# Optimization experiments

Hardware: AMD Instinct MI355X
Metric: run time of the kernel (lower is better)

The kernel has to match this reference:

```python
import jax, jax.numpy as jnp
import numpy as np

KC = 32      # cluster_num
KS = 3       # kernel_size
AREA = KS * KS
ITERS = 10   # KMeans Lloyd iterations (fixed, deterministic init)


def _unfold3(x):
    # torch nn.Unfold(kernel_size=3, padding=1): feature dim ordered cin-major, area-minor
    b, c, h, w = x.shape
    xp = jnp.pad(x, ((0, 0), (0, 0), (1, 1), (1, 1)))
    cols = jnp.stack([xp[:, :, i:i + h, j:j + w] for i in range(KS) for j in range(KS)], axis=2)  # [b,c,area,h,w]
    return cols.reshape(b, c * AREA, h * w).transpose(0, 2, 1)  # [b, hw, c*area]


def _kmeans_assign(feat):
    # Lloyd's KMeans on [s, d] features; deterministic strided init; returns [s] int assignments
    s, d = feat.shape
    c0 = feat[jnp.arange(KC) * (s // KC)]
    f2 = (feat * feat).sum(-1, keepdims=True)
    def dists(c):
        return f2 - 2.0 * feat @ c.T + (c * c).sum(-1)[None, :]
    def step(c, _):
        idx = jnp.argmin(dists(c), axis=1)
        cnt = jax.ops.segment_sum(jnp.ones((s,), feat.dtype), idx, KC)
        sm = jax.ops.segment_sum(feat, idx, KC)
        c_new = jnp.where(cnt[:, None] > 0, sm / jnp.maximum(cnt, 1.0)[:, None], c)
        return c_new, None
    c, _ = jax.lax.scan(step, c0, None, length=ITERS)
    return jnp.argmin(dists(c), axis=1)


def _seg_mean(p, idx):
    # per-cluster mean of patches -> patch-space centroids [K, f]
    s = p.shape[0]
    cnt = jax.ops.segment_sum(jnp.ones((s,), p.dtype), idx, KC)
    return jax.ops.segment_sum(p, idx, KC) / jnp.maximum(cnt, 1.0)[:, None]


def _mlp2(x, W1, b1, W2, b2):
    return jax.nn.relu(jax.nn.relu(x @ W1 + b1) @ W2 + b2)


def setup_inputs():
    key = jax.random.key(0)
    ks = jax.random.split(key, 16)
    cin, cout, m = 32, 32, 16
    f = cin * AREA
    g = lambda k, shp, sc: jax.random.normal(k, shp, dtype=jnp.float32) * sc
    return {
        "x": g(ks[0], (4, cin, 64, 64), 1.0),
        "Wh1": g(ks[1], (f, m), (2.0 / f) ** 0.5), "bh1": jnp.zeros((m,), jnp.float32),
        "Wh2": g(ks[2], (m, m), (2.0 / m) ** 0.5), "bh2": jnp.zeros((m,), jnp.float32),
        "Wa": g(ks[3], (m, AREA), (2.0 / m) ** 0.5), "ba": jnp.zeros((AREA,), jnp.float32),
        "Wc": g(ks[4], (m, cin), (2.0 / m) ** 0.5), "bc": jnp.zeros((cin,), jnp.float32),
        "Wo": g(ks[5], (m, cout), (2.0 / m) ** 0.5), "bo": jnp.zeros((cout,), jnp.float32),
        "kernels": g(ks[6], (cin, AREA, cout), (2.0 / (cin * AREA)) ** 0.5),
        "Wb1": g(ks[7], (f, m), (2.0 / f) ** 0.5), "bb1": jnp.zeros((m,), jnp.float32),
        "Wb2": g(ks[8], (m, m), (2.0 / m) ** 0.5), "bb2": jnp.zeros((m,), jnp.float32),
        "Wb3": g(ks[9], (m, cout), (2.0 / m) ** 0.5), "bb3": jnp.zeros((cout,), jnp.float32),
    }


def reference(x, Wh1, bh1, Wh2, bh2, Wa, ba, Wc, bc, Wo, bo, kernels, Wb1, bb1, Wb2, bb2, Wb3, bb3):
    b, cin, h, w = x.shape
    s = h * w
    cout = kernels.shape[-1]
    patches = _unfold3(x)                                        # [b, s, cin*area]
    feat = patches.reshape(b, s, cin, AREA).mean(-1)             # cluster_source='channel'
    idx = jax.vmap(_kmeans_assign)(jax.lax.stop_gradient(feat))  # [b, s] cluster assignments
    centroids = jax.vmap(_seg_mean)(patches, idx)                # [b, K, cin*area]
    # low_rank kernel generator: rank-1 modulation along cin/area/cout of shared base kernel
    kf = _mlp2(centroids, Wh1, bh1, Wh2, bh2)                    # [b, K, m]
    w_cin = jax.nn.sigmoid(kf @ Wc + bc)                         # [b, K, cin]
    w_area = jax.nn.sigmoid(kf @ Wa + ba)                        # [b, K, area]
    w_cout = jax.nn.sigmoid(kf @ Wo + bo)                        # [b, K, cout]
    kern = (w_cin[:, :, :, None, None] * w_area[:, :, None, :, None]
            * w_cout[:, :, None, None, :] * kernels[None, None])  # [b, K, cin, area, cout]
    kern = kern.reshape(b, KC, cin * AREA, cout)
    bias = _mlp2(centroids, Wb1, bb1, Wb2, bb2) @ Wb3 + bb3      # [b, K, cout] (bias='cluster')
    # gather per-pixel kernel/bias by cluster id, grouped matmul, scatter back (dense-gather form)
    bi = jnp.arange(b)[:, None]
    Wpix = kern[bi, idx]                                         # [b, s, f, cout]
    out = jnp.einsum('bsf,bsfo->bso', patches, Wpix) + bias[bi, idx]
    return out.reshape(b, h, w, cout).transpose(0, 3, 1, 2), idx
```

## Files before the change

kernel.cpp:

```cpp
#include <hip/hip_runtime.h>
#include <stdint.h>

typedef unsigned long long u64;

#define Bn 4
#define CINn 32
#define Hn 64
#define Wn 64
#define Sn 4096
#define KCn 32
#define Mn 16
#define COUTn 32
#define AREAn 9
#define Fn 288
#define NITER 10
#define FXSCALE 4294967296.0
#define SPLITn 4

static __device__ __forceinline__ float relu_(float v){ return v > 0.f ? v : 0.f; }
static __device__ __forceinline__ float sigm_(float v){ return 1.f / (1.f + __expf(-v) * 0.f + expf(-v) * 1.f); }
static __device__ __forceinline__ float sigmoid_(float v){ return 1.f / (1.f + expf(-v)); }

__global__ __launch_bounds__(256) void k_feat(const float* __restrict__ x,
                                              float* __restrict__ feat,
                                              u64* __restrict__ gsum,
                                              unsigned* __restrict__ gcnt){
    int g = blockIdx.x * 256 + threadIdx.x;
    if (g < 3 * Bn * KCn * CINn) gsum[g] = 0ull;
    if (g < 3 * Bn * KCn)        gcnt[g] = 0u;
    int p = g & (Sn - 1);
    int c = (g >> 12) & (CINn - 1);
    int b = g >> 17;
    int y = p >> 6, xx = p & 63;
    const float* xc = x + ((size_t)(b * CINn + c) << 12);
    float s = 0.f;
    #pragma unroll
    for (int i = 0; i < 3; ++i){
        int yy = y + i - 1;
        if (yy < 0 || yy >= Hn) continue;
        #pragma unroll
        for (int j = 0; j < 3; ++j){
            int xj = xx + j - 1;
            if (xj < 0 || xj >= Wn) continue;
            s += xc[(yy << 6) + xj];
        }
    }
    feat[g] = s * (1.f / 9.f);
}

__global__ __launch_bounds__(256) void k_assign(const float* __restrict__ feat,
                                                float* __restrict__ gcent,
                                                u64* __restrict__ gsum,
                                                unsigned* __restrict__ gcnt,
                                                int* __restrict__ idx,
                                                float* __restrict__ idxf,
                                                int iter){
    __shared__ float cent[KCn][CINn];
    __shared__ float c2[KCn];
    __shared__ u64   lsum[KCn][CINn];
    __shared__ unsigned lcnt[KCn];

    int tid  = threadIdx.x;
    int b    = blockIdx.x >> 4;
    int tile = blockIdx.x & 15;
    int prev = (iter + 2) % 3;
    int cur  = iter % 3;
    int nxt  = (iter + 1) % 3;

    for (int e = tid; e < KCn * CINn; e += 256){
        int k = e >> 5, c = e & 31;
        float v;
        if (iter == 0){
            v = feat[(b * CINn + c) * Sn + k * (Sn / KCn)];
        } else {
            u64 svu     = gsum[((prev * Bn + b) * KCn + k) * CINn + c];
            unsigned cn = gcnt[(prev * Bn + b) * KCn + k];
            if (cn > 0) v = (float)((double)(long long)svu / ((double)cn * FXSCALE));
            else        v = gcent[(b * KCn + k) * CINn + c];
        }
        cent[k][c] = v;
        lsum[k][c] = 0ull;
        if (tile == 0){
            gcent[(b * KCn + k) * CINn + c] = v;
            gsum[((nxt * Bn + b) * KCn + k) * CINn + c] = 0ull;
        }
    }
    for (int e = tid; e < KCn; e += 256){
        lcnt[e] = 0u;
        if (tile == 0) gcnt[(nxt * Bn + b) * KCn + e] = 0u;
    }
    __syncthreads();
    if (tid < KCn){
        float s = 0.f;
        #pragma unroll
        for (int c = 0; c < CINn; ++c) s += cent[tid][c] * cent[tid][c];
        c2[tid] = s;
    }
    __syncthreads();

    int p = (tile << 8) | tid;
    float fv[CINn];
    #pragma unroll
    for (int c = 0; c < CINn; ++c) fv[c] = feat[(b * CINn + c) * Sn + p];
    float f2 = 0.f;
    #pragma unroll
    for (int c = 0; c < CINn; ++c) f2 = fmaf(fv[c], fv[c], f2);

    float best = 3.402823466e38f; int bi = 0;
    #pragma unroll 4
    for (int k = 0; k < KCn; ++k){
        float dot = 0.f;
        #pragma unroll
        for (int c = 0; c < CINn; ++c) dot = fmaf(fv[c], cent[k][c], dot);
        float d = f2 - 2.f * dot + c2[k];
        if (d < best){ best = d; bi = k; }
    }

    if (iter == NITER){
        idx[b * Sn + p]  = bi;
        idxf[b * Sn + p] = (float)bi;
        return;
    }

    atomicAdd(&lcnt[bi], 1u);
    #pragma unroll
    for (int c = 0; c < CINn; ++c){
        long long q = llrint((double)fv[c] * FXSCALE);
        atomicAdd(&lsum[bi][c], (u64)q);
    }
    __syncthreads();
    for (int e = tid; e < KCn * CINn; e += 256){
        int k = e >> 5, c = e & 31;
        u64 v = lsum[k][c];
        if (v) atomicAdd(&gsum[((cur * Bn + b) * KCn + k) * CINn + c], v);
    }
    if (tid < KCn){
        unsigned v = lcnt[tid];
        if (v) atomicAdd(&gcnt[(cur * Bn + b) * KCn + tid], v);
    }
}

__global__ __launch_bounds__(256) void k_sort(const int* __restrict__ idx,
                                              int* __restrict__ sorted,
                                              int* __restrict__ offs){
    int b = blockIdx.x, tid = threadIdx.x;
    __shared__ unsigned hist[256][KCn];
    __shared__ unsigned cnts[KCn];
    __shared__ unsigned baseK[KCn + 1];
    #pragma unroll
    for (int k = 0; k < KCn; ++k) hist[tid][k] = 0u;
    int p0 = tid * 16;
    int myk[16];
    #pragma unroll
    for (int i = 0; i < 16; ++i){
        int k = idx[b * Sn + p0 + i];
        myk[i] = k;
        hist[tid][k]++;
    }
    __syncthreads();
    if (tid < KCn){
        unsigned run = 0;
        for (int t = 0; t < 256; ++t){ unsigned v = hist[t][tid]; hist[t][tid] = run; run += v; }
        cnts[tid] = run;
    }
    __syncthreads();
    if (tid == 0){
        unsigned acc = 0;
        for (int k = 0; k < KCn; ++k){ baseK[k] = acc; acc += cnts[k]; }
        baseK[KCn] = acc;
    }
    __syncthreads();
    if (tid <= KCn) offs[b * (KCn + 1) + tid] = (int)baseK[tid];
    #pragma unroll
    for (int i = 0; i < 16; ++i){
        int k = myk[i];
        unsigned pos = baseK[k] + hist[tid][k];
        hist[tid][k]++;
        sorted[b * Sn + pos] = p0 + i;
    }
}

__global__ __launch_bounds__(320) void k_segsum(const float* __restrict__ x,
                                                const int* __restrict__ sorted,
                                                const int* __restrict__ offs,
                                                float* __restrict__ centp){
    int bk = blockIdx.x; int b = bk >> 5; int k = bk & 31;
    int tid = threadIdx.x;
    int f = tid < Fn ? tid : (Fn - 1);
    int off0 = offs[b * (KCn + 1) + k];
    int n    = offs[b * (KCn + 1) + k + 1] - off0;
    int c = f / 9, a = f - c * 9;
    int di = a / 3 - 1, dj = a % 3 - 1;
    const float* xc = x + ((size_t)(b * CINn + c) << 12);
    const int* plist = sorted + b * Sn + off0;
    __shared__ int pl[320];
    float sum = 0.f;
    for (int base = 0; base < n; base += 320){
        int m = min(320, n - base);
        __syncthreads();
        if (tid < m) pl[tid] = plist[base + tid];
        __syncthreads();
        #pragma unroll 4
        for (int i = 0; i < m; ++i){
            int p = pl[i];
            int y = (p >> 6) + di, xx = (p & 63) + dj;
            float v = (y >= 0 && y < Hn && xx >= 0 && xx < Wn) ? xc[(y << 6) + xx] : 0.f;
            sum += v;
        }
    }
    if (tid < Fn) centp[(b * KCn + k) * Fn + f] = sum / (float)max(n, 1);
}

__global__ __launch_bounds__(512) void k_mlp(const float* __restrict__ centp,
        const float* __restrict__ Wh1, const float* __restrict__ bh1,
        const float* __restrict__ Wh2, const float* __restrict__ bh2,
        const float* __restrict__ Wa,  const float* __restrict__ ba,
        const float* __restrict__ Wc,  const float* __restrict__ bc,
        const float* __restrict__ Wo,  const float* __restrict__ bo,
        const float* __restrict__ Wb1, const float* __restrict__ bb1,
        const float* __restrict__ Wb2, const float* __restrict__ bb2,
        const float* __restrict__ Wb3, const float* __restrict__ bb3,
        float* __restrict__ wcin, float* __restrict__ warea,
        float* __restrict__ wcout, float* __restrict__ biasb){
    int b = blockIdx.x, tid = threadIdx.x;
    int k = tid >> 4, j = tid & 15;
    __shared__ float centL[KCn * Fn];
    __shared__ float h1[KCn][Mn], hb1s[KCn][Mn];
    __shared__ float kf[KCn][Mn], hb2[KCn][Mn];
    for (int e = tid; e < KCn * Fn; e += 512) centL[e] = centp[b * KCn * Fn + e];
    __syncthreads();
    {
        float a1 = bh1[j], a2 = bb1[j];
        const float* cr = centL + k * Fn;
        for (int f = 0; f < Fn; ++f){
            float cv = cr[f];
            a1 = fmaf(cv, Wh1[f * Mn + j], a1);
            a2 = fmaf(cv, Wb1[f * Mn + j], a2);
        }
        h1[k][j]   = relu_(a1);
        hb1s[k][j] = relu_(a2);
    }
    __syncthreads();
    {
        float a1 = bh2[j], a2 = bb2[j];
        #pragma unroll
        for (int i = 0; i < Mn; ++i){
            a1 = fmaf(h1[k][i],   Wh2[i * Mn + j], a1);
            a2 = fmaf(hb1s[k][i], Wb2[i * Mn + j], a2);
        }
        kf[k][j]  = relu_(a1);
        hb2[k][j] = relu_(a2);
    }
    __syncthreads();
    for (int e = tid; e < KCn * COUTn; e += 512){
        int kk = e >> 5, o = e & 31;
        float s1 = bc[o], s2 = bo[o], s3 = bb3[o];
        #pragma unroll
        for (int i = 0; i < Mn; ++i){
            float kv = kf[kk][i];
            s1 = fmaf(kv, Wc[i * COUTn + o], s1);
            s2 = fmaf(kv, Wo[i * COUTn + o], s2);
            s3 = fmaf(hb2[kk][i], Wb3[i * COUTn + o], s3);
        }
        wcin [(b * KCn + kk) * CINn  + o] = sigmoid_(s1);
        wcout[(b * KCn + kk) * COUTn + o] = sigmoid_(s2);
        biasb[(b * KCn + kk) * COUTn + o] = s3;
    }
    if (tid < KCn * AREAn){
        int kk = tid / 9, a = tid - kk * 9;
        float s = ba[a];
        #pragma unroll
        for (int i = 0; i < Mn; ++i) s = fmaf(kf[kk][i], Wa[i * AREAn + a], s);
        warea[(b * KCn + kk) * AREAn + a] = sigmoid_(s);
    }
}

__global__ __launch_bounds__(256) void k_out(const float* __restrict__ x,
                                             const int* __restrict__ sorted,
                                             const int* __restrict__ offs,
                                             const float* __restrict__ wcin,
                                             const float* __restrict__ warea,
                                             const float* __restrict__ wcout,
                                             const float* __restrict__ biasb,
                                             const float* __restrict__ kern0,
                                             float* __restrict__ out){
    int g  = blockIdx.x;
    int sp = g & (SPLITn - 1);
    int k  = (g >> 2) & 31;
    int b  = g >> 7;
    int tid = threadIdx.x;

    __shared__ float kernT[COUTn][292];
    __shared__ float biasL[COUTn];
    __shared__ float wcl[CINn], wal[16], wol[COUTn];
    __shared__ float patchL[8 * Fn];
    __shared__ int   pix[8];

    if (tid < 32)                 wcl[tid]       = wcin [(b * KCn + k) * CINn  + tid];
    else if (tid < 64)            wol[tid - 32]  = wcout[(b * KCn + k) * COUTn + tid - 32];
    else if (tid < 64 + AREAn)    wal[tid - 64]  = warea[(b * KCn + k) * AREAn + tid - 64];
    else if (tid >= 96 && tid < 128) biasL[tid - 96] = biasb[(b * KCn + k) * COUTn + tid - 96];
    __syncthreads();

    for (int e = tid; e < Fn * COUTn; e += 256){
        int f = e >> 5, o = e & 31;
        int c = f / 9, a = f - c * 9;
        kernT[o][f] = wcl[c] * wal[a] * wol[o] * kern0[e];
    }

    int off0 = offs[b * (KCn + 1) + k];
    int n    = offs[b * (KCn + 1) + k + 1] - off0;
    int per  = (n + SPLITn - 1) >> 2;
    int i0 = sp * per, i1 = min(n, i0 + per);
    __syncthreads();

    for (int base = i0; base < i1; base += 8){
        int m = min(8, i1 - base);
        if (tid < 8) pix[tid] = (tid < m) ? sorted[b * Sn + off0 + base + tid] : -1;
        __syncthreads();
        for (int v = tid; v < 8 * Fn; v += 256){
            int pl = v / Fn, f = v - pl * Fn;
            int p = pix[pl];
            float val = 0.f;
            if (p >= 0){
                int c = f / 9, a = f - c * 9;
                int y = (p >> 6) + a / 3 - 1, xx = (p & 63) + (a % 3) - 1;
                if (y >= 0 && y < Hn && xx >= 0 && xx < Wn)
                    val = x[((size_t)(b * CINn + c) << 12) + (y << 6) + xx];
            }
            patchL[v] = val;
        }
        __syncthreads();
        int pl = tid >> 5, o = tid & 31;
        if (pl < m){
            const float* pr = patchL + pl * Fn;
            const float* kr = &kernT[o][0];
            float a0 = 0.f, a1 = 0.f, a2 = 0.f, a3 = 0.f;
            #pragma unroll
            for (int f = 0; f < Fn; f += 4){
                float4 pv = *reinterpret_cast<const float4*>(pr + f);
                float4 kv = *reinterpret_cast<const float4*>(kr + f);
                a0 = fmaf(pv.x, kv.x, a0);
                a1 = fmaf(pv.y, kv.y, a1);
                a2 = fmaf(pv.z, kv.z, a2);
                a3 = fmaf(pv.w, kv.w, a3);
            }
            float acc = biasL[o] + ((a0 + a1) + (a2 + a3));
            out[((size_t)(b * COUTn + o) << 12) + pix[pl]] = acc;
        }
        __syncthreads();
    }
}

extern "C" void kernel_launch(void* const* d_in, const int* in_sizes, int n_in,
                              void* d_out, int out_size, void* d_ws, size_t ws_size,
                              hipStream_t stream){
    const float* x    = (const float*)d_in[0];
    const float* Wh1  = (const float*)d_in[1];
    const float* bh1  = (const float*)d_in[2];
    const float* Wh2  = (const float*)d_in[3];
    const float* bh2  = (const float*)d_in[4];
    const float* Wa   = (const float*)d_in[5];
    const float* ba   = (const float*)d_in[6];
    const float* Wc   = (const float*)d_in[7];
    const float* bc   = (const float*)d_in[8];
    const float* Wo   = (const float*)d_in[9];
    const float* bo   = (const float*)d_in[10];
    const float* kern0= (const float*)d_in[11];
    const float* Wb1  = (const float*)d_in[12];
    const float* bb1  = (const float*)d_in[13];
    const float* Wb2  = (const float*)d_in[14];
    const float* bb2  = (const float*)d_in[15];
    const float* Wb3  = (const float*)d_in[16];
    const float* bb3  = (const float*)d_in[17];

    char* ws = (char*)d_ws;
    float*    feat   = (float*)(ws + 0);
    float*    gcent  = (float*)(ws + 2097152);
    u64*      gsum   = (u64*)  (ws + 2113536);
    unsigned* gcnt   = (unsigned*)(ws + 2211840);
    int*      idx    = (int*)  (ws + 2213376);
    int*      sorted = (int*)  (ws + 2278912);
    int*      offs   = (int*)  (ws + 2344448);
    float*    centp  = (float*)(ws + 2345216);
    float*    wcin   = (float*)(ws + 2492672);
    float*    warea  = (float*)(ws + 2509056);
    float*    wcout  = (float*)(ws + 2513664);
    float*    biasb  = (float*)(ws + 2530048);

    float* outp = (float*)d_out;
    float* idxf = outp + (size_t)Bn * COUTn * Sn;

    k_feat<<<(Bn * CINn * Sn) / 256, 256, 0, stream>>>(x, feat, gsum, gcnt);
    for (int it = 0; it <= NITER; ++it)
        k_assign<<<Bn * 16, 256, 0, stream>>>(feat, gcent, gsum, gcnt, idx, idxf, it);
    k_sort<<<Bn, 256, 0, stream>>>(idx, sorted, offs);
    k_segsum<<<Bn * KCn, 320, 0, stream>>>(x, sorted, offs, centp);
    k_mlp<<<Bn, 512, 0, stream>>>(centp, Wh1, bh1, Wh2, bh2, Wa, ba, Wc, bc, Wo, bo,
                                  Wb1, bb1, Wb2, bb2, Wb3, bb3,
                                  wcin, warea, wcout, biasb);
    k_out<<<Bn * KCn * SPLITn, 256, 0, stream>>>(x, sorted, offs, wcin, warea, wcout,
                                                 biasb, kern0, outp);
}
```

Baseline: 248.2 us.

## Fuse KMeans iterations, sort, segsum and MLP into one persistent kernel with grid barriers

The separate per-iteration assign launches, the sort, the segment-sum and the MLP kernels are merged into one persistent kernel with 32 blocks per batch. The blocks synchronise through a software atomic barrier, which removes about 14 kernel launches and their serialization gaps. The per-cluster sums are now built in shared memory by bucketing pixels into lists rather than doing 64-bit shared atomics per channel, and each block splits the 32 centroid distance checks across two half-blocks. The output kernel is retiled to fixed 32-pixel tiles with 2x2 register blocking and rebuilds the kernel for each cluster run, which risks redundant kernel builds and depends on all blocks being co-resident for the spin barrier.

```diff
diff --git a/kernel.cpp b/kernel.cpp
--- a/kernel.cpp
+++ b/kernel.cpp
@@ -15,19 +15,39 @@
 #define Fn 288
 #define NITER 10
 #define FXSCALE 4294967296.0
-#define SPLITn 4
+#define NBLK_B 32
+#define LDK 292
 
 static __device__ __forceinline__ float relu_(float v){ return v > 0.f ? v : 0.f; }
-static __device__ __forceinline__ float sigm_(float v){ return 1.f / (1.f + __expf(-v) * 0.f + expf(-v) * 1.f); }
 static __device__ __forceinline__ float sigmoid_(float v){ return 1.f / (1.f + expf(-v)); }
 
-__global__ __launch_bounds__(256) void k_feat(const float* __restrict__ x,
+static __device__ __forceinline__ void batch_barrier(unsigned* bar){
+    __syncthreads();
+    if (threadIdx.x == 0){
+        unsigned* cnt = bar;
+        unsigned* gen = bar + 16;
+        unsigned g = __hip_atomic_load(gen, __ATOMIC_RELAXED, __HIP_MEMORY_SCOPE_AGENT);
+        unsigned a = __hip_atomic_fetch_add(cnt, 1u, __ATOMIC_ACQ_REL, __HIP_MEMORY_SCOPE_AGENT);
+        if (a == (unsigned)(NBLK_B - 1)){
+            __hip_atomic_store(cnt, 0u, __ATOMIC_RELAXED, __HIP_MEMORY_SCOPE_AGENT);
+            __hip_atomic_fetch_add(gen, 1u, __ATOMIC_RELEASE, __HIP_MEMORY_SCOPE_AGENT);
+        } else {
+            while (__hip_atomic_load(gen, __ATOMIC_ACQUIRE, __HIP_MEMORY_SCOPE_AGENT) == g)
+                __builtin_amdgcn_s_sleep(4);
+        }
+    }
+    __syncthreads();
+}
+
+__global__ __launch_bounds__(256) void k_init(const float* __restrict__ x,
                                               float* __restrict__ feat,
                                               u64* __restrict__ gsum,
-                                              unsigned* __restrict__ gcnt){
+                                              unsigned* __restrict__ gcnt,
+                                              unsigned* __restrict__ bar){
     int g = blockIdx.x * 256 + threadIdx.x;
     if (g < 3 * Bn * KCn * CINn) gsum[g] = 0ull;
     if (g < 3 * Bn * KCn)        gcnt[g] = 0u;
+    if (g < 4 * 32)              bar[g]  = 0u;
     int p = g & (Sn - 1);
     int c = (g >> 12) & (CINn - 1);
     int b = g >> 17;
@@ -48,170 +68,36 @@
     feat[g] = s * (1.f / 9.f);
 }
 
-__global__ __launch_bounds__(256) void k_assign(const float* __restrict__ feat,
-                                                float* __restrict__ gcent,
-                                                u64* __restrict__ gsum,
-                                                unsigned* __restrict__ gcnt,
-                                                int* __restrict__ idx,
-                                                float* __restrict__ idxf,
-                                                int iter){
-    __shared__ float cent[KCn][CINn];
-    __shared__ float c2[KCn];
-    __shared__ u64   lsum[KCn][CINn];
-    __shared__ unsigned lcnt[KCn];
-
-    int tid  = threadIdx.x;
-    int b    = blockIdx.x >> 4;
-    int tile = blockIdx.x & 15;
-    int prev = (iter + 2) % 3;
-    int cur  = iter % 3;
-    int nxt  = (iter + 1) % 3;
-
-    for (int e = tid; e < KCn * CINn; e += 256){
-        int k = e >> 5, c = e & 31;
-        float v;
-        if (iter == 0){
-            v = feat[(b * CINn + c) * Sn + k * (Sn / KCn)];
-        } else {
-            u64 svu     = gsum[((prev * Bn + b) * KCn + k) * CINn + c];
-            unsigned cn = gcnt[(prev * Bn + b) * KCn + k];
-            if (cn > 0) v = (float)((double)(long long)svu / ((double)cn * FXSCALE));
-            else        v = gcent[(b * KCn + k) * CINn + c];
-        }
-        cent[k][c] = v;
-        lsum[k][c] = 0ull;
-        if (tile == 0){
-            gcent[(b * KCn + k) * CINn + c] = v;
-            gsum[((nxt * Bn + b) * KCn + k) * CINn + c] = 0ull;
-        }
-    }
-    for (int e = tid; e < KCn; e += 256){
-        lcnt[e] = 0u;
-        if (tile == 0) gcnt[(nxt * Bn + b) * KCn + e] = 0u;
-    }
-    __syncthreads();
-    if (tid < KCn){
-        float s = 0.f;
-        #pragma unroll
-        for (int c = 0; c < CINn; ++c) s += cent[tid][c] * cent[tid][c];
-        c2[tid] = s;
-    }
-    __syncthreads();
-
-    int p = (tile << 8) | tid;
-    float fv[CINn];
-    #pragma unroll
-    for (int c = 0; c < CINn; ++c) fv[c] = feat[(b * CINn + c) * Sn + p];
-    float f2 = 0.f;
-    #pragma unroll
-    for (int c = 0; c < CINn; ++c) f2 = fmaf(fv[c], fv[c], f2);
-
-    float best = 3.402823466e38f; int bi = 0;
-    #pragma unroll 4
-    for (int k = 0; k < KCn; ++k){
-        float dot = 0.f;
-        #pragma unroll
-        for (int c = 0; c < CINn; ++c) dot = fmaf(fv[c], cent[k][c], dot);
-        float d = f2 - 2.f * dot + c2[k];
-        if (d < best){ best = d; bi = k; }
-    }
-
-    if (iter == NITER){
-        idx[b * Sn + p]  = bi;
-        idxf[b * Sn + p] = (float)bi;
-        return;
-    }
-
-    atomicAdd(&lcnt[bi], 1u);
-    #pragma unroll
-    for (int c = 0; c < CINn; ++c){
-        long long q = llrint((double)fv[c] * FXSCALE);
-        atomicAdd(&lsum[bi][c], (u64)q);
-    }
-    __syncthreads();
-    for (int e = tid; e < KCn * CINn; e += 256){
-        int k = e >> 5, c = e & 31;
-        u64 v = lsum[k][c];
-        if (v) atomicAdd(&gsum[((cur * Bn + b) * KCn + k) * CINn + c], v);
-    }
-    if (tid < KCn){
-        unsigned v = lcnt[tid];
-        if (v) atomicAdd(&gcnt[(cur * Bn + b) * KCn + tid], v);
-    }
-}
-
-__global__ __launch_bounds__(256) void k_sort(const int* __restrict__ idx,
-                                              int* __restrict__ sorted,
-                                              int* __restrict__ offs){
-    int b = blockIdx.x, tid = threadIdx.x;
-    __shared__ unsigned hist[256][KCn];
-    __shared__ unsigned cnts[KCn];
-    __shared__ unsigned baseK[KCn + 1];
-    #pragma unroll
-    for (int k = 0; k < KCn; ++k) hist[tid][k] = 0u;
-    int p0 = tid * 16;
-    int myk[16];
-    #pragma unroll
-    for (int i = 0; i < 16; ++i){
-        int k = idx[b * Sn + p0 + i];
-        myk[i] = k;
-        hist[tid][k]++;
-    }
-    __syncthreads();
-    if (tid < KCn){
-        unsigned run = 0;
-        for (int t = 0; t < 256; ++t){ unsigned v = hist[t][tid]; hist[t][tid] = run; run += v; }
-        cnts[tid] = run;
-    }
-    __syncthreads();
-    if (tid == 0){
-        unsigned acc = 0;
-        for (int k = 0; k < KCn; ++k){ baseK[k] = acc; acc += cnts[k]; }
-        baseK[KCn] = acc;
-    }
-    __syncthreads();
-    if (tid <= KCn) offs[b * (KCn + 1) + tid] = (int)baseK[tid];
-    #pragma unroll
-    for (int i = 0; i < 16; ++i){
-        int k = myk[i];
-        unsigned pos = baseK[k] + hist[tid][k];
-        hist[tid][k]++;
-        sorted[b * Sn + pos] = p0 + i;
-    }
-}
-
-__global__ __launch_bounds__(320) void k_segsum(const float* __restrict__ x,
-                                                const int* __restrict__ sorted,
-                                                const int* __restrict__ offs,
-                                                float* __restrict__ centp){
-    int bk = blockIdx.x; int b = bk >> 5; int k = bk & 31;
-    int tid = threadIdx.x;
-    int f = tid < Fn ? tid : (Fn - 1);
-    int off0 = offs[b * (KCn + 1) + k];
-    int n    = offs[b * (KCn + 1) + k + 1] - off0;
-    int c = f / 9, a = f - c * 9;
-    int di = a / 3 - 1, dj = a % 3 - 1;
-    const float* xc = x + ((size_t)(b * CINn + c) << 12);
-    const int* plist = sorted + b * Sn + off0;
-    __shared__ int pl[320];
-    float sum = 0.f;
-    for (int base = 0; base < n; base += 320){
-        int m = min(320, n - base);
-        __syncthreads();
-        if (tid < m) pl[tid] = plist[base + tid];
-        __syncthreads();
-        #pragma unroll 4
-        for (int i = 0; i < m; ++i){
-            int p = pl[i];
-            int y = (p >> 6) + di, xx = (p & 63) + dj;
-            float v = (y >= 0 && y < Hn && xx >= 0 && xx < Wn) ? xc[(y << 6) + xx] : 0.f;
-            sum += v;
-        }
-    }
-    if (tid < Fn) centp[(b * KCn + k) * Fn + f] = sum / (float)max(n, 1);
-}
-
-__global__ __launch_bounds__(512) void k_mlp(const float* __restrict__ centp,
+struct AssignSh {
+    u64   fxL[128][32];
+    float cent[KCn][CINn];
+    float c2[KCn];
+    float bestd[256];
+    int   bestk[256];
+    unsigned cnt32[KCn];
+    unsigned base32[KCn + 1];
+    unsigned scat[KCn];
+    int   plist[128];
+};
+struct SortSh {
+    unsigned hist[256][KCn];
+    unsigned cnts[KCn];
+    unsigned baseK[KCn + 1];
+};
+struct SmkSh {
+    float centL[Fn];
+    int   pl[256];
+    float part1[16][16], part2[16][16];
+    float hL[2][Mn];
+    float kfL[2][Mn];
+};
+union ShU { AssignSh a; SortSh s; SmkSh m; };
+
+__global__ __launch_bounds__(256) void k_main(const float* __restrict__ x,
+        const float* __restrict__ feat,
+        float* __restrict__ gcent, u64* __restrict__ gsum, unsigned* __restrict__ gcnt,
+        int* __restrict__ idx, float* __restrict__ idxf,
+        int* __restrict__ sorted, int* __restrict__ offs,
         const float* __restrict__ Wh1, const float* __restrict__ bh1,
         const float* __restrict__ Wh2, const float* __restrict__ bh2,
         const float* __restrict__ Wa,  const float* __restrict__ ba,
@@ -221,134 +107,378 @@
         const float* __restrict__ Wb2, const float* __restrict__ bb2,
         const float* __restrict__ Wb3, const float* __restrict__ bb3,
         float* __restrict__ wcin, float* __restrict__ warea,
-        float* __restrict__ wcout, float* __restrict__ biasb){
-    int b = blockIdx.x, tid = threadIdx.x;
-    int k = tid >> 4, j = tid & 15;
-    __shared__ float centL[KCn * Fn];
-    __shared__ float h1[KCn][Mn], hb1s[KCn][Mn];
-    __shared__ float kf[KCn][Mn], hb2[KCn][Mn];
-    for (int e = tid; e < KCn * Fn; e += 512) centL[e] = centp[b * KCn * Fn + e];
-    __syncthreads();
+        float* __restrict__ wcout, float* __restrict__ biasb,
+        unsigned* __restrict__ bars){
+    __shared__ ShU sh;
+    int tid  = threadIdx.x;
+    int b    = blockIdx.x >> 5;
+    int tnum = blockIdx.x & 31;
+    unsigned* bar = bars + b * 32;
+
+    int pxi  = tid & 127;
+    int half = tid >> 7;
+    int p    = tnum * 128 + pxi;
+
+    float fv[CINn];
+    #pragma unroll
+    for (int c = 0; c < CINn; ++c) fv[c] = feat[(b * CINn + c) * Sn + p];
+    float f2 = 0.f;
+    #pragma unroll
+    for (int c = 0; c < CINn; ++c) f2 = fmaf(fv[c], fv[c], f2);
+
+    if (tid < 128){
+        #pragma unroll
+        for (int c = 0; c < CINn; ++c)
+            sh.a.fxL[tid][c] = (u64)llrint((double)fv[c] * FXSCALE);
+    }
+
+    for (int iter = 0; iter <= NITER; ++iter){
+        int prev = (iter + 2) % 3;
+        int cur  = iter % 3;
+        int nxt  = (iter + 1) % 3;
+
+        for (int e = tid; e < KCn * CINn; e += 256){
+            int k = e >> 5, c = e & 31;
+            float v;
+            if (iter == 0){
+                v = feat[(b * CINn + c) * Sn + k * (Sn / KCn)];
+            } else {
+                u64 sv     = gsum[((prev * Bn + b) * KCn + k) * CINn + c];
+                unsigned cn = gcnt[(prev * Bn + b) * KCn + k];
+                if (cn > 0) v = (float)((double)(long long)sv / ((double)cn * FXSCALE));
+                else        v = gcent[(b * KCn + k) * CINn + c];
+            }
+            sh.a.cent[k][c] = v;
+            if (tnum == 0){
+                gcent[(b * KCn + k) * CINn + c] = v;
+                gsum[((nxt * Bn + b) * KCn + k) * CINn + c] = 0ull;
+            }
+        }
+        if (tnum == 0 && tid < KCn) gcnt[(nxt * Bn + b) * KCn + tid] = 0u;
+        __syncthreads();
+        if (tid < 32){
+            float s = 0.f;
+            #pragma unroll
+            for (int c = 0; c < CINn; ++c) s = fmaf(sh.a.cent[tid][c], sh.a.cent[tid][c], s);
+            sh.a.c2[tid] = s;
+        } else if (tid < 64){
+            sh.a.cnt32[tid - 32] = 0u;
+        } else if (tid < 96){
+            sh.a.scat[tid - 64] = 0u;
+        }
+        __syncthreads();
+
+        float best = 3.402823466e38f;
+        int   bk   = half * 16;
+        #pragma unroll 4
+        for (int k = 0; k < 16; ++k){
+            int kk = half * 16 + k;
+            const float* cr = sh.a.cent[kk];
+            float dot = 0.f;
+            #pragma unroll
+            for (int c = 0; c < CINn; ++c) dot = fmaf(fv[c], cr[c], dot);
+            float d = f2 - 2.f * dot + sh.a.c2[kk];
+            if (d < best){ best = d; bk = kk; }
+        }
+        sh.a.bestd[tid] = best;
+        sh.a.bestk[tid] = bk;
+        __syncthreads();
+
+        int bi = -1;
+        if (tid < 128){
+            float d0 = sh.a.bestd[tid], d1 = sh.a.bestd[tid + 128];
+            int   k0 = sh.a.bestk[tid], k1 = sh.a.bestk[tid + 128];
+            bi = (d1 < d0) ? k1 : k0;
+            if (iter == NITER){
+                idx[b * Sn + p]  = bi;
+                idxf[b * Sn + p] = (float)bi;
+            } else {
+                atomicAdd(&sh.a.cnt32[bi], 1u);
+            }
+        }
+
+        if (iter < NITER){
+            __syncthreads();
+            if (tid == 0){
+                unsigned acc = 0;
+                #pragma unroll
+                for (int k = 0; k < KCn; ++k){ sh.a.base32[k] = acc; acc += sh.a.cnt32[k]; }
+                sh.a.base32[KCn] = acc;
+            }
+            __syncthreads();
+            if (tid < 128){
+                unsigned pos = sh.a.base32[bi] + atomicAdd(&sh.a.scat[bi], 1u);
+                sh.a.plist[pos] = tid;
+            }
+            __syncthreads();
+            {
+                int k  = tid >> 3;
+                int cg = (tid & 7) * 4;
+                unsigned s0 = sh.a.base32[k];
+                unsigned nk = sh.a.cnt32[k];
+                u64 a0 = 0, a1 = 0, a2 = 0, a3 = 0;
+                for (unsigned i = 0; i < nk; ++i){
+                    int px = sh.a.plist[s0 + i];
+                    a0 += sh.a.fxL[px][cg + 0];
+                    a1 += sh.a.fxL[px][cg + 1];
+                    a2 += sh.a.fxL[px][cg + 2];
+                    a3 += sh.a.fxL[px][cg + 3];
+                }
+                u64* gs = &gsum[((cur * Bn + b) * KCn + k) * CINn + cg];
+                if (a0) atomicAdd(gs + 0, a0);
+                if (a1) atomicAdd(gs + 1, a1);
+                if (a2) atomicAdd(gs + 2, a2);
+                if (a3) atomicAdd(gs + 3, a3);
+                if ((tid & 7) == 0 && nk) atomicAdd(&gcnt[(cur * Bn + b) * KCn + k], nk);
+            }
+        }
+        batch_barrier(bar);
+    }
+
+    if (tnum == 0){
+        #pragma unroll
+        for (int k = 0; k < KCn; ++k) sh.s.hist[tid][k] = 0u;
+        int p0 = tid * 16;
+        int myk[16];
+        #pragma unroll
+        for (int i = 0; i < 16; ++i){
+            int k = idx[b * Sn + p0 + i];
+            myk[i] = k;
+            sh.s.hist[tid][k]++;
+        }
+        __syncthreads();
+        if (tid < KCn){
+            unsigned run = 0;
+            for (int t2 = 0; t2 < 256; ++t2){ unsigned v = sh.s.hist[t2][tid]; sh.s.hist[t2][tid] = run; run += v; }
+            sh.s.cnts[tid] = run;
+        }
+        __syncthreads();
+        if (tid == 0){
+            unsigned acc = 0;
+            for (int k = 0; k < KCn; ++k){ sh.s.baseK[k] = acc; acc += sh.s.cnts[k]; }
+            sh.s.baseK[KCn] = acc;
+        }
+        __syncthreads();
+        if (tid <= KCn) offs[b * (KCn + 1) + tid] = (int)sh.s.baseK[tid];
+        #pragma unroll
+        for (int i = 0; i < 16; ++i){
+            int k = myk[i];
+            unsigned pos = sh.s.baseK[k] + sh.s.hist[tid][k];
+            sh.s.hist[tid][k]++;
+            sorted[b * Sn + pos] = p0 + i;
+        }
+    }
+    batch_barrier(bar);
+
+    int kk = tnum;
+    int off0 = offs[b * (KCn + 1) + kk];
+    int n    = offs[b * (KCn + 1) + kk + 1] - off0;
+
     {
-        float a1 = bh1[j], a2 = bb1[j];
-        const float* cr = centL + k * Fn;
-        for (int f = 0; f < Fn; ++f){
-            float cv = cr[f];
-            a1 = fmaf(cv, Wh1[f * Mn + j], a1);
-            a2 = fmaf(cv, Wb1[f * Mn + j], a2);
-        }
-        h1[k][j]   = relu_(a1);
-        hb1s[k][j] = relu_(a2);
-    }
-    __syncthreads();
+        int fA = tid;           int cA = fA / 9, aA = fA - cA * 9;
+        int dyA = aA / 3 - 1,   dxA = aA % 3 - 1;
+        int fB = 256 + tid;     int cB = fB / 9, aB = fB - cB * 9;
+        int dyB = aB / 3 - 1,   dxB = aB % 3 - 1;
+        float sumA = 0.f, sumB = 0.f;
+        for (int base = 0; base < n; base += 256){
+            int m = min(256, n - base);
+            __syncthreads();
+            if (tid < m) sh.m.pl[tid] = sorted[b * Sn + off0 + base + tid];
+            __syncthreads();
+            for (int i = 0; i < m; ++i){
+                int pp = sh.m.pl[i];
+                int py = pp >> 6, px2 = pp & 63;
+                int y1 = py + dyA, x1 = px2 + dxA;
+                float v = (y1 >= 0 && y1 < Hn && x1 >= 0 && x1 < Wn)
+                          ? x[((size_t)(b * CINn + cA) << 12) + (y1 << 6) + x1] : 0.f;
+                sumA += v;
+                if (tid < 32){
+                    int y2 = py + dyB, x2 = px2 + dxB;
+                    float v2 = (y2 >= 0 && y2 < Hn && x2 >= 0 && x2 < Wn)
+                               ? x[((size_t)(b * CINn + cB) << 12) + (y2 << 6) + x2] : 0.f;
+                    sumB += v2;
+                }
+            }
+        }
+        __syncthreads();
+        float inv = 1.f / (float)max(n, 1);
+        sh.m.centL[fA] = sumA * (float)max(n,1) * 0.f + sumA / (float)max(n, 1);
+        (void)inv;
+        if (tid < 32) sh.m.centL[fB] = sumB / (float)max(n, 1);
+    }
+    __syncthreads();
+
     {
-        float a1 = bh2[j], a2 = bb2[j];
+        int j = tid & 15, rep = tid >> 4;
+        float p1 = 0.f, p2 = 0.f;
+        int fbeg = rep * 18;
+        for (int ff = fbeg; ff < fbeg + 18; ++ff){
+            float cv = sh.m.centL[ff];
+            p1 = fmaf(cv, Wh1[ff * Mn + j], p1);
+            p2 = fmaf(cv, Wb1[ff * Mn + j], p2);
+        }
+        sh.m.part1[rep][j] = p1;
+        sh.m.part2[rep][j] = p2;
+    }
+    __syncthreads();
+    if (tid < 32){
+        int br = tid >> 4, j = tid & 15;
+        float s = br ? bb1[j] : bh1[j];
+        for (int r = 0; r < 16; ++r) s += br ? sh.m.part2[r][j] : sh.m.part1[r][j];
+        sh.m.hL[br][j] = relu_(s);
+    }
+    __syncthreads();
+    if (tid < 32){
+        int br = tid >> 4, j = tid & 15;
+        const float* W2 = br ? Wb2 : Wh2;
+        float s = br ? bb2[j] : bh2[j];
+        #pragma unroll
+        for (int i = 0; i < Mn; ++i) s = fmaf(sh.m.hL[br][i], W2[i * Mn + j], s);
+        sh.m.kfL[br][j] = relu_(s);
+    }
+    __syncthreads();
+    if (tid < 32){
+        int o = tid;
+        float s1 = bc[o], s2 = bo[o], s3 = bb3[o];
         #pragma unroll
         for (int i = 0; i < Mn; ++i){
-            a1 = fmaf(h1[k][i],   Wh2[i * Mn + j], a1);
-            a2 = fmaf(hb1s[k][i], Wb2[i * Mn + j], a2);
-        }
-        kf[k][j]  = relu_(a1);
-        hb2[k][j] = relu_(a2);
-    }
-    __syncthreads();
-    for (int e = tid; e < KCn * COUTn; e += 512){
-        int kk = e >> 5, o = e & 31;
-        float s1 = bc[o], s2 = bo[o], s3 = bb3[o];
-        #pragma unroll
-        for (int i = 0; i < Mn; ++i){
-            float kv = kf[kk][i];
+            float kv = sh.m.kfL[0][i];
             s1 = fmaf(kv, Wc[i * COUTn + o], s1);
             s2 = fmaf(kv, Wo[i * COUTn + o], s2);
-            s3 = fmaf(hb2[kk][i], Wb3[i * COUTn + o], s3);
+            s3 = fmaf(sh.m.kfL[1][i], Wb3[i * COUTn + o], s3);
         }
         wcin [(b * KCn + kk) * CINn  + o] = sigmoid_(s1);
         wcout[(b * KCn + kk) * COUTn + o] = sigmoid_(s2);
         biasb[(b * KCn + kk) * COUTn + o] = s3;
-    }
-    if (tid < KCn * AREAn){
-        int kk = tid / 9, a = tid - kk * 9;
-        float s = ba[a];
-        #pragma unroll
-        for (int i = 0; i < Mn; ++i) s = fmaf(kf[kk][i], Wa[i * AREAn + a], s);
-        warea[(b * KCn + kk) * AREAn + a] = sigmoid_(s);
+    } else if (tid < 41){
+        int a2 = tid - 32;
+        float s = ba[a2];
+        #pragma unroll
+        for (int i = 0; i < Mn; ++i) s = fmaf(sh.m.kfL[0][i], Wa[i * AREAn + a2], s);
+        warea[(b * KCn + kk) * AREAn + a2] = sigmoid_(s);
     }
 }
 
 __global__ __launch_bounds__(256) void k_out(const float* __restrict__ x,
                                              const int* __restrict__ sorted,
-                                             const int* __restrict__ offs,
+                                             const int* __restrict__ idx,
                                              const float* __restrict__ wcin,
                                              const float* __restrict__ warea,
                                              const float* __restrict__ wcout,
                                              const float* __restrict__ biasb,
                                              const float* __restrict__ kern0,
                                              float* __restrict__ out){
-    int g  = blockIdx.x;
-    int sp = g & (SPLITn - 1);
-    int k  = (g >> 2) & 31;
-    int b  = g >> 7;
-    int tid = threadIdx.x;
-
-    __shared__ float kernT[COUTn][292];
-    __shared__ float biasL[COUTn];
-    __shared__ float wcl[CINn], wal[16], wol[COUTn];
-    __shared__ float patchL[8 * Fn];
-    __shared__ int   pix[8];
-
-    if (tid < 32)                 wcl[tid]       = wcin [(b * KCn + k) * CINn  + tid];
-    else if (tid < 64)            wol[tid - 32]  = wcout[(b * KCn + k) * COUTn + tid - 32];
-    else if (tid < 64 + AREAn)    wal[tid - 64]  = warea[(b * KCn + k) * AREAn + tid - 64];
-    else if (tid >= 96 && tid < 128) biasL[tid - 96] = biasb[(b * KCn + k) * COUTn + tid - 96];
-    __syncthreads();
-
-    for (int e = tid; e < Fn * COUTn; e += 256){
-        int f = e >> 5, o = e & 31;
-        int c = f / 9, a = f - c * 9;
-        kernT[o][f] = wcl[c] * wal[a] * wol[o] * kern0[e];
-    }
-
-    int off0 = offs[b * (KCn + 1) + k];
-    int n    = offs[b * (KCn + 1) + k + 1] - off0;
-    int per  = (n + SPLITn - 1) >> 2;
-    int i0 = sp * per, i1 = min(n, i0 + per);
-    __syncthreads();
-
-    for (int base = i0; base < i1; base += 8){
-        int m = min(8, i1 - base);
-        if (tid < 8) pix[tid] = (tid < m) ? sorted[b * Sn + off0 + base + tid] : -1;
-        __syncthreads();
-        for (int v = tid; v < 8 * Fn; v += 256){
-            int pl = v / Fn, f = v - pl * Fn;
-            int p = pix[pl];
-            float val = 0.f;
-            if (p >= 0){
-                int c = f / 9, a = f - c * 9;
-                int y = (p >> 6) + a / 3 - 1, xx = (p & 63) + (a % 3) - 1;
-                if (y >= 0 && y < Hn && xx >= 0 && xx < Wn)
-                    val = x[((size_t)(b * CINn + c) << 12) + (y << 6) + xx];
-            }
-            patchL[v] = val;
-        }
-        __syncthreads();
-        int pl = tid >> 5, o = tid & 31;
-        if (pl < m){
-            const float* pr = patchL + pl * Fn;
-            const float* kr = &kernT[o][0];
-            float a0 = 0.f, a1 = 0.f, a2 = 0.f, a3 = 0.f;
-            #pragma unroll
-            for (int f = 0; f < Fn; f += 4){
-                float4 pv = *reinterpret_cast<const float4*>(pr + f);
-                float4 kv = *reinterpret_cast<const float4*>(kr + f);
-                a0 = fmaf(pv.x, kv.x, a0);
-                a1 = fmaf(pv.y, kv.y, a1);
-                a2 = fmaf(pv.z, kv.z, a2);
-                a3 = fmaf(pv.w, kv.w, a3);
-            }
-            float acc = biasL[o] + ((a0 + a1) + (a2 + a3));
-            out[((size_t)(b * COUTn + o) << 12) + pix[pl]] = acc;
-        }
-        __syncthreads();
+    int b    = blockIdx.x >> 7;
+    int tile = blockIdx.x & 127;
+    int tid  = threadIdx.x;
+
+    __shared__ float kernT[KCn * LDK];
+    __shared__ float patchL[32 * LDK];
+    __shared__ int   pix[32];
+    __shared__ int   kid[32];
+    __shared__ float wcl[CINn], wal[AREAn], wol[COUTn], biasL[COUTn];
+
+    if (tid < 32){
+        int pp = sorted[b * Sn + tile * 32 + tid];
+        pix[tid] = pp;
+        kid[tid] = idx[b * Sn + pp];
+    }
+    int fA = tid;       int cA = fA / 9, aA = fA - cA * 9;
+    int dyA = aA / 3 - 1, dxA = aA % 3 - 1;
+    int fB = 256 + tid; int cB = fB / 9, aB = fB - cB * 9;
+    int dyB = aB / 3 - 1, dxB = aB % 3 - 1;
+    __syncthreads();
+
+    #pragma unroll 4
+    for (int px = 0; px < 32; ++px){
+        int pp = pix[px];
+        int py = pp >> 6, pxx = pp & 63;
+        int y1 = py + dyA, x1 = pxx + dxA;
+        patchL[px * LDK + tid] = (y1 >= 0 && y1 < Hn && x1 >= 0 && x1 < Wn)
+            ? x[((size_t)(b * CINn + cA) << 12) + (y1 << 6) + x1] : 0.f;
+        if (tid < 32){
+            int y2 = py + dyB, x2 = pxx + dxB;
+            patchL[px * LDK + 256 + tid] = (y2 >= 0 && y2 < Hn && x2 >= 0 && x2 < Wn)
+                ? x[((size_t)(b * CINn + cB) << 12) + (y2 << 6) + x2] : 0.f;
+        }
+    }
+
+    int o2 = tid & 15, p2 = tid >> 4;
+    int oA = o2 * 2, oB = o2 * 2 + 1;
+    int pxA = p2 * 2, pxB = p2 * 2 + 1;
+
+    int i0 = 0;
+    while (i0 < 32){
+        __syncthreads();
+        int kcur = kid[i0];
+        int i1 = i0 + 1;
+        while (i1 < 32 && kid[i1] == kcur) ++i1;
+
+        if (tid < 32)       wcl[tid]        = wcin [(b * KCn + kcur) * CINn  + tid];
+        else if (tid < 64)  wol[tid - 32]   = wcout[(b * KCn + kcur) * COUTn + tid - 32];
+        else if (tid < 73)  wal[tid - 64]   = warea[(b * KCn + kcur) * AREAn + tid - 64];
+        else if (tid >= 96 && tid < 128) biasL[tid - 96] = biasb[(b * KCn + kcur) * COUTn + tid - 96];
+        __syncthreads();
+
+        {
+            int o  = tid >> 3;
+            int q  = tid & 7;
+            int f0 = q * 36;
+            int cc = q * 4, aa = 0;
+            float wo_ = wol[o];
+            float* kr = kernT + o * LDK + f0;
+            #pragma unroll 4
+            for (int i2 = 0; i2 < 36; ++i2){
+                kr[i2] = wcl[cc] * wal[aa] * wo_ * kern0[(f0 + i2) * COUTn + o];
+                if (++aa == 9){ aa = 0; ++cc; }
+            }
+        }
+        __syncthreads();
+
+        bool actA = (pxA >= i0 && pxA < i1);
+        bool actB = (pxB >= i0 && pxB < i1);
+        if (actA || actB){
+            const float* krA = kernT + oA * LDK;
+            const float* krB = kernT + oB * LDK;
+            const float* prA = patchL + pxA * LDK;
+            const float* prB = patchL + pxB * LDK;
+            float s00 = 0.f, s01 = 0.f, s10 = 0.f, s11 = 0.f;
+            if (actA && actB){
+                #pragma unroll 4
+                for (int fq = 0; fq < Fn; fq += 4){
+                    float4 k0 = *reinterpret_cast<const float4*>(krA + fq);
+                    float4 k1 = *reinterpret_cast<const float4*>(krB + fq);
+                    float4 pa = *reinterpret_cast<const float4*>(prA + fq);
+                    float4 pb = *reinterpret_cast<const float4*>(prB + fq);
+                    s00 = fmaf(pa.x,k0.x,s00); s00 = fmaf(pa.y,k0.y,s00); s00 = fmaf(pa.z,k0.z,s00); s00 = fmaf(pa.w,k0.w,s00);
+                    s01 = fmaf(pa.x,k1.x,s01); s01 = fmaf(pa.y,k1.y,s01); s01 = fmaf(pa.z,k1.z,s01); s01 = fmaf(pa.w,k1.w,s01);
+                    s10 = fmaf(pb.x,k0.x,s10); s10 = fmaf(pb.y,k0.y,s10); s10 = fmaf(pb.z,k0.z,s10); s10 = fmaf(pb.w,k0.w,s10);
+                    s11 = fmaf(pb.x,k1.x,s11); s11 = fmaf(pb.y,k1.y,s11); s11 = fmaf(pb.z,k1.z,s11); s11 = fmaf(pb.w,k1.w,s11);
+                }
+            } else {
+                const float* pr = actA ? prA : prB;
+                #pragma unroll 4
+                for (int fq = 0; fq < Fn; fq += 4){
+                    float4 k0 = *reinterpret_cast<const float4*>(krA + fq);
+                    float4 k1 = *reinterpret_cast<const float4*>(krB + fq);
+                    float4 pa = *reinterpret_cast<const float4*>(pr + fq);
+                    s00 = fmaf(pa.x,k0.x,s00); s00 = fmaf(pa.y,k0.y,s00); s00 = fmaf(pa.z,k0.z,s00); s00 = fmaf(pa.w,k0.w,s00);
+                    s01 = fmaf(pa.x,k1.x,s01); s01 = fmaf(pa.y,k1.y,s01); s01 = fmaf(pa.z,k1.z,s01); s01 = fmaf(pa.w,k1.w,s01);
+                }
+                if (actB){ s10 = s00; s11 = s01; s00 = 0.f; s01 = 0.f; }
+            }
+            if (actA){
+                int pp = pix[pxA];
+                out[((size_t)(b * COUTn + oA) << 12) + pp] = biasL[oA] + s00;
+                out[((size_t)(b * COUTn + oB) << 12) + pp] = biasL[oB] + s01;
+            }
+            if (actB){
+                int pp = pix[pxB];
+                out[((size_t)(b * COUTn + oA) << 12) + pp] = biasL[oA] + s10;
+                out[((size_t)(b * COUTn + oB) << 12) + pp] = biasL[oB] + s11;
+            }
+        }
+        i0 = i1;
     }
 }
 
@@ -376,29 +506,27 @@
 
     char* ws = (char*)d_ws;
     float*    feat   = (float*)(ws + 0);
-    float*    gcent  = (float*)(ws + 2097152);
-    u64*      gsum   = (u64*)  (ws + 2113536);
-    unsigned* gcnt   = (unsigned*)(ws + 2211840);
+    u64*      gsum   = (u64*)  (ws + 2097152);
+    unsigned* gcnt   = (unsigned*)(ws + 2195456);
+    float*    gcent  = (float*)(ws + 2196992);
     int*      idx    = (int*)  (ws + 2213376);
     int*      sorted = (int*)  (ws + 2278912);
     int*      offs   = (int*)  (ws + 2344448);
-    float*    centp  = (float*)(ws + 2345216);
-    float*    wcin   = (float*)(ws + 2492672);
-    float*    warea  = (float*)(ws + 2509056);
-    float*    wcout  = (float*)(ws + 2513664);
-    float*    biasb  = (float*)(ws + 2530048);
+    float*    wcin   = (float*)(ws + 2345472);
+    float*    warea  = (float*)(ws + 2361856);
+    float*    wcout  = (float*)(ws + 2366464);
+    float*    biasb  = (float*)(ws + 2382848);
+    unsigned* bars   = (unsigned*)(ws + 2399232);
 
     float* outp = (float*)d_out;
     float* idxf = outp + (size_t)Bn * COUTn * Sn;
 
-    k_feat<<<(Bn * CINn * Sn) / 256, 256, 0, stream>>>(x, feat, gsum, gcnt);
-    for (int it = 0; it <= NITER; ++it)
-        k_assign<<<Bn * 16, 256, 0, stream>>>(feat, gcent, gsum, gcnt, idx, idxf, it);
-    k_sort<<<Bn, 256, 0, stream>>>(idx, sorted, offs);
-    k_segsum<<<Bn * KCn, 320, 0, stream>>>(x, sorted, offs, centp);
-    k_mlp<<<Bn, 512, 0, stream>>>(centp, Wh1, bh1, Wh2, bh2, Wa, ba, Wc, bc, Wo, bo,
-                                  Wb1, bb1, Wb2, bb2, Wb3, bb3,
-                                  wcin, warea, wcout, biasb);
-    k_out<<<Bn * KCn * SPLITn, 256, 0, stream>>>(x, sorted, offs, wcin, warea, wcout,
-                                                 biasb, kern0, outp);
+    k_init<<<(Bn * CINn * Sn) / 256, 256, 0, stream>>>(x, feat, gsum, gcnt, bars);
+    k_main<<<Bn * NBLK_B, 256, 0, stream>>>(x, feat, gcent, gsum, gcnt, idx, idxf,
+                                            sorted, offs,
+                                            Wh1, bh1, Wh2, bh2, Wa, ba, Wc, bc, Wo, bo,
+                                            Wb1, bb1, Wb2, bb2, Wb3, bb3,
+                                            wcin, warea, wcout, biasb, bars);
+    k_out<<<Bn * 128, 256, 0, stream>>>(x, sorted, idx, wcin, warea, wcout, biasb,
+                                        kern0, outp);
 }
```

New measurement: 308.6 us. 1.24x slower.
